# Performance work log

Measured on AMD Instinct MI355X. Metric: run time of the kernel, lower is better.

The kernel has to match this reference:

```python
import jax, jax.numpy as jnp
import numpy as np

INPUT_SIZE = 512
HIDDEN = 1024
NUM_CLASSES = 1000
BATCH = 64
SEQ = 512


def setup_inputs() -> dict:
    key = jax.random.key(0)
    ks = jax.random.split(key, 12)
    comb = INPUT_SIZE + HIDDEN
    s = 1.0 / np.sqrt(comb)
    sf = 1.0 / np.sqrt(HIDDEN)
    return {
        "x": jax.random.normal(ks[0], (BATCH, SEQ, INPUT_SIZE), dtype=jnp.float32),
        "Wz_w": jax.random.uniform(ks[1], (HIDDEN, comb), jnp.float32, -s, s),
        "Wz_b": jax.random.uniform(ks[2], (HIDDEN,), jnp.float32, -s, s),
        "Wr_w": jax.random.uniform(ks[3], (HIDDEN, comb), jnp.float32, -s, s),
        "Wr_b": jax.random.uniform(ks[4], (HIDDEN,), jnp.float32, -s, s),
        "Wc_w": jax.random.uniform(ks[5], (HIDDEN, comb), jnp.float32, -s, s),
        "Wc_b": jax.random.uniform(ks[6], (HIDDEN,), jnp.float32, -s, s),
        "Wo_w": jax.random.uniform(ks[7], (HIDDEN, comb), jnp.float32, -s, s),
        "Wo_b": jax.random.uniform(ks[8], (HIDDEN,), jnp.float32, -s, s),
        "fc_w": jax.random.uniform(ks[9], (NUM_CLASSES, HIDDEN), jnp.float32, -sf, sf),
        "fc_b": jax.random.uniform(ks[10], (NUM_CLASSES,), jnp.float32, -sf, sf),
    }


def reference(x, Wz_w, Wz_b, Wr_w, Wr_b, Wc_w, Wc_b, Wo_w, Wo_b, fc_w, fc_b):
    B, T, _ = x.shape
    H = Wz_w.shape[0]

    def step(carry, x_t):
        h, c = carry
        combined = jnp.concatenate([x_t, h], axis=1)          # [B, I+H]
        z = jax.nn.sigmoid(combined @ Wz_w.T + Wz_b)
        r = jax.nn.sigmoid(combined @ Wr_w.T + Wr_b)
        combined_reset = jnp.concatenate([x_t, r * c], axis=1)
        c_tilde = jnp.tanh(combined_reset @ Wc_w.T + Wc_b)
        c_new = z * c + (1.0 - z) * c_tilde
        o = jax.nn.sigmoid(combined @ Wo_w.T + Wo_b)
        h_new = o * jnp.tanh(c_new)
        return (h_new, c_new), None

    h0 = jnp.zeros((B, H), dtype=x.dtype)
    c0 = jnp.zeros((B, H), dtype=x.dtype)
    xs = jnp.swapaxes(x, 0, 1)                                # [T, B, I]
    (h, c), _ = jax.lax.scan(step, (h0, c0), xs)
    # dropout is identity (p=0 / eval mode)
    return h @ fc_w.T + fc_b                                  # [B, num_classes]
```

## Files before the change

kernel.cpp:

```cpp
#include <hip/hip_runtime.h>

#define NWG 128
#define TSTEPS 512

typedef __attribute__((ext_vector_type(8))) short short8;
typedef __attribute__((ext_vector_type(4))) float f32x4;

#define T0_OFF   0
#define T1_OFF   49152
#define T2_OFF   98304
#define RED_OFF  131072
#define ZBUF_OFF 135168
#define OBUF_OFF 137216
#define XCB_OFF  139264
#define CST_OFF  141312
#define RCS_OFF  143360
#define HST_OFF  145408
#define BIAS_OFF 147456
#define LDS_BYTES 147584

__device__ inline unsigned short f2bf(float f) {
  unsigned int b = __float_as_uint(f);
  return (unsigned short)((b + 0x7FFFu + ((b >> 16) & 1u)) >> 16);
}
__device__ inline float sigm(float x) { return 1.f / (1.f + __expf(-x)); }
__device__ inline float tanh_f(float x) { float e = __expf(2.f * x); return 1.f - 2.f / (e + 1.f); }

__device__ inline void cstore16(void* p, short8 v) {
  asm volatile("global_store_dwordx4 %0, %1, off sc0 sc1" :: "v"(p), "v"(v) : "memory");
}
__device__ inline void cstore4(void* p, int v) {
  asm volatile("global_store_dword %0, %1, off sc0 sc1" :: "v"(p), "v"(v) : "memory");
}
__device__ inline int cload4(const void* p) {
  int v;
  asm volatile("global_load_dword %0, %1, off sc0 sc1\n\ts_waitcnt vmcnt(0)"
               : "=&v"(v) : "v"(p) : "memory");
  return v;
}
__device__ inline void vmdrain() {
  asm volatile("s_waitcnt vmcnt(0)" ::: "memory");
}

__device__ inline void cload24(const unsigned short* p0, const unsigned short* p1, short8* a) {
  asm volatile(
    "global_load_dwordx4 %0,  %24, off sc0 sc1\n\t"
    "global_load_dwordx4 %1,  %24, off offset:64 sc0 sc1\n\t"
    "global_load_dwordx4 %2,  %24, off offset:128 sc0 sc1\n\t"
    "global_load_dwordx4 %3,  %24, off offset:192 sc0 sc1\n\t"
    "global_load_dwordx4 %4,  %24, off offset:256 sc0 sc1\n\t"
    "global_load_dwordx4 %5,  %24, off offset:320 sc0 sc1\n\t"
    "global_load_dwordx4 %6,  %24, off offset:384 sc0 sc1\n\t"
    "global_load_dwordx4 %7,  %24, off offset:448 sc0 sc1\n\t"
    "global_load_dwordx4 %8,  %24, off offset:512 sc0 sc1\n\t"
    "global_load_dwordx4 %9,  %24, off offset:576 sc0 sc1\n\t"
    "global_load_dwordx4 %10, %24, off offset:640 sc0 sc1\n\t"
    "global_load_dwordx4 %11, %24, off offset:704 sc0 sc1\n\t"
    "global_load_dwordx4 %12, %24, off offset:768 sc0 sc1\n\t"
    "global_load_dwordx4 %13, %24, off offset:832 sc0 sc1\n\t"
    "global_load_dwordx4 %14, %24, off offset:896 sc0 sc1\n\t"
    "global_load_dwordx4 %15, %24, off offset:960 sc0 sc1\n\t"
    "global_load_dwordx4 %16, %25, off sc0 sc1\n\t"
    "global_load_dwordx4 %17, %25, off offset:64 sc0 sc1\n\t"
    "global_load_dwordx4 %18, %25, off offset:128 sc0 sc1\n\t"
    "global_load_dwordx4 %19, %25, off offset:192 sc0 sc1\n\t"
    "global_load_dwordx4 %20, %25, off offset:256 sc0 sc1\n\t"
    "global_load_dwordx4 %21, %25, off offset:320 sc0 sc1\n\t"
    "global_load_dwordx4 %22, %25, off offset:384 sc0 sc1\n\t"
    "global_load_dwordx4 %23, %25, off offset:448 sc0 sc1\n\t"
    "s_waitcnt vmcnt(0)"
    : "=&v"(a[0]), "=&v"(a[1]), "=&v"(a[2]), "=&v"(a[3]),
      "=&v"(a[4]), "=&v"(a[5]), "=&v"(a[6]), "=&v"(a[7]),
      "=&v"(a[8]), "=&v"(a[9]), "=&v"(a[10]), "=&v"(a[11]),
      "=&v"(a[12]), "=&v"(a[13]), "=&v"(a[14]), "=&v"(a[15]),
      "=&v"(a[16]), "=&v"(a[17]), "=&v"(a[18]), "=&v"(a[19]),
      "=&v"(a[20]), "=&v"(a[21]), "=&v"(a[22]), "=&v"(a[23])
    : "v"(p0), "v"(p1)
    : "memory");
}

__device__ inline void cload16(const unsigned short* p, short8* a) {
  asm volatile(
    "global_load_dwordx4 %0,  %16, off sc0 sc1\n\t"
    "global_load_dwordx4 %1,  %16, off offset:64 sc0 sc1\n\t"
    "global_load_dwordx4 %2,  %16, off offset:128 sc0 sc1\n\t"
    "global_load_dwordx4 %3,  %16, off offset:192 sc0 sc1\n\t"
    "global_load_dwordx4 %4,  %16, off offset:256 sc0 sc1\n\t"
    "global_load_dwordx4 %5,  %16, off offset:320 sc0 sc1\n\t"
    "global_load_dwordx4 %6,  %16, off offset:384 sc0 sc1\n\t"
    "global_load_dwordx4 %7,  %16, off offset:448 sc0 sc1\n\t"
    "global_load_dwordx4 %8,  %16, off offset:512 sc0 sc1\n\t"
    "global_load_dwordx4 %9,  %16, off offset:576 sc0 sc1\n\t"
    "global_load_dwordx4 %10, %16, off offset:640 sc0 sc1\n\t"
    "global_load_dwordx4 %11, %16, off offset:704 sc0 sc1\n\t"
    "global_load_dwordx4 %12, %16, off offset:768 sc0 sc1\n\t"
    "global_load_dwordx4 %13, %16, off offset:832 sc0 sc1\n\t"
    "global_load_dwordx4 %14, %16, off offset:896 sc0 sc1\n\t"
    "global_load_dwordx4 %15, %16, off offset:960 sc0 sc1\n\t"
    "s_waitcnt vmcnt(0)"
    : "=&v"(a[0]), "=&v"(a[1]), "=&v"(a[2]), "=&v"(a[3]),
      "=&v"(a[4]), "=&v"(a[5]), "=&v"(a[6]), "=&v"(a[7]),
      "=&v"(a[8]), "=&v"(a[9]), "=&v"(a[10]), "=&v"(a[11]),
      "=&v"(a[12]), "=&v"(a[13]), "=&v"(a[14]), "=&v"(a[15])
    : "v"(p)
    : "memory");
}

__global__ void __launch_bounds__(256) lmgru_kernel(
    const float* __restrict__ x,
    const float* __restrict__ Wz, const float* __restrict__ bz,
    const float* __restrict__ Wr, const float* __restrict__ br,
    const float* __restrict__ Wc, const float* __restrict__ bc,
    const float* __restrict__ Wo, const float* __restrict__ bo,
    const float* __restrict__ fcw, const float* __restrict__ fcb,
    float* __restrict__ out, char* __restrict__ ws)
{
  extern __shared__ char lds[];
  const int tid  = threadIdx.x;
  const int wg   = blockIdx.x;
  const int lane = tid & 63;
  const int q    = tid >> 6;

  unsigned short* hbuf  = (unsigned short*)ws;
  unsigned short* rcbuf = (unsigned short*)(ws + 262144);
  unsigned short* xring = (unsigned short*)(ws + 524288);
  float*          h32   = (float*)(ws + 655360);
  int* hflagA  = (int*)(ws + 917504);
  int* hflagB  = hflagA + 128;
  int* rcflagA = hflagA + 256;
  int* rcflagB = hflagA + 384;
  int* hflag[2]  = {hflagA, hflagB};
  int* rcflag[2] = {rcflagA, rcflagB};

  float* zbuf = (float*)(lds + ZBUF_OFF);
  float* obuf = (float*)(lds + OBUF_OFF);
  float* xcb  = (float*)(lds + XCB_OFF);
  float* cst  = (float*)(lds + CST_OFF);
  float* rcs  = (float*)(lds + RCS_OFF);
  float* hst  = (float*)(lds + HST_OFF);
  float* bias = (float*)(lds + BIAS_OFF);

  const float* Wg[4] = {Wz, Wr, Wo, Wc};

  for (int it = 0; it < 12; ++it) {
    int slot = tid + 256 * it;
    int s = slot >> 6, l = slot & 63;
    int nn = l & 15, kg = (l >> 4) & 3;
    int k = 32 * s + kg * 8;
    int g = (nn < 8) ? 0 : 1;
    const float* src = Wg[g] + (8 * wg + (nn & 7)) * 1536 + k;
    short8 pk;
    #pragma unroll
    for (int j = 0; j < 8; ++j) pk[j] = (short)f2bf(src[j]);
    *(short8*)(lds + T0_OFF + s * 1024 + l * 16) = pk;
  }
  for (int it = 0; it < 12; ++it) {
    int slot = tid + 256 * it;
    int s = slot >> 6, l = slot & 63;
    int nn = l & 15, kg = (l >> 4) & 3;
    int k = 32 * s + kg * 8;
    int g = (nn < 8) ? 2 : 3;
    short8 pk = {};
    if (g == 2 || k < 512) {
      const float* src = Wg[g] + (8 * wg + (nn & 7)) * 1536 + k;
      #pragma unroll
      for (int j = 0; j < 8; ++j) pk[j] = (short)f2bf(src[j]);
    }
    *(short8*)(lds + T1_OFF + s * 1024 + l * 16) = pk;
  }
  for (int it = 0; it < 8; ++it) {
    int slot = tid + 256 * it;
    int s = slot >> 6, l = slot & 63;
    int nn = l & 15, kg = (l >> 4) & 3;
    int k = 32 * s + kg * 8;
    short8 pk = {};
    if (nn < 8) {
      const float* src = Wc + (8 * wg + nn) * 1536 + 512 + k;
      #pragma unroll
      for (int j = 0; j < 8; ++j) pk[j] = (short)f2bf(src[j]);
    }
    *(short8*)(lds + T2_OFF + s * 1024 + l * 16) = pk;
  }
  if (tid < 32) {
    const float* Bg[4] = {bz, br, bo, bc};
    bias[tid] = Bg[tid >> 3][8 * wg + (tid & 7)];
  }
  cst[tid] = 0.f; cst[tid + 256] = 0.f;
  if (tid < 64) {
    short8 z8 = {};
    cstore16(hbuf + tid * 1024 + 8 * wg, z8);
  }
  if (tid < 32) {
    int e = wg * 256 + tid * 8;
    int b = e >> 9, f = e & 511;
    const float* xs = x + b * 262144 + f;
    short8 pk;
    #pragma unroll
    for (int j = 0; j < 8; ++j) pk[j] = (short)f2bf(xs[j]);
    cstore16(xring + 32768 + b * 512 + f, pk);
  }
  __syncthreads();
  if (tid == 0) {
    vmdrain();
    cstore4(&hflagA[wg], 0);
    cstore4(&hflagB[wg], 0);
    cstore4(&rcflagA[wg], 0);
    cstore4(&rcflagB[wg], 0);
  }

  const int m   = q & 1;
  const int kh  = q >> 1;
  const int nn  = lane & 15;
  const int kg8 = ((lane >> 4) & 3) * 8;
  const int rbase = ((lane >> 4) & 3) * 4;

  for (int t = 1; t <= TSTEPS; ++t) {
    const int pc = t & 1, pp = (t - 1) & 1;

    for (int X = 0; X < 2; ++X) {
      if (tid < 128) {
        const int* fp = &hflag[X][tid];
        while (cload4(fp) < t - 1) __builtin_amdgcn_s_sleep(1);
      }
      __syncthreads();

      const int bbase = 32 * X;
      const int brow  = bbase + 16 * m + nn;
      f32x4 acc0 = {0.f, 0.f, 0.f, 0.f}, acc1 = {0.f, 0.f, 0.f, 0.f};
      const unsigned short* xr = xring + pc * 32768 + brow * 512;
      const unsigned short* hb = hbuf + pp * 65536 + brow * 1024;
      const unsigned short* p0 = kh ? (hb + 256 + kg8) : (xr + kg8);
      const unsigned short* p1 = kh ? (hb + 768 + kg8) : (hb + kg8);
      short8 af[24];
      cload24(p0, p1, af);
      #pragma unroll
      for (int j = 0; j < 24; ++j) {
        int s = 24 * kh + j;
        short8 b0 = *(const short8*)(lds + T0_OFF + s * 1024 + lane * 16);
        short8 b1 = *(const short8*)(lds + T1_OFF + s * 1024 + lane * 16);
        acc0 = __builtin_amdgcn_mfma_f32_16x16x32_bf16(af[j], b0, acc0, 0, 0, 0);
        acc1 = __builtin_amdgcn_mfma_f32_16x16x32_bf16(af[j], b1, acc1, 0, 0, 0);
      }
      if (kh == 1) {
        *(f32x4*)(lds + RED_OFF + ((m * 2 + 0) * 64 + lane) * 16) = acc0;
        *(f32x4*)(lds + RED_OFF + ((m * 2 + 1) * 64 + lane) * 16) = acc1;
      }
      __syncthreads();
      if (kh == 0) {
        acc0 += *(const f32x4*)(lds + RED_OFF + ((m * 2 + 0) * 64 + lane) * 16);
        acc1 += *(const f32x4*)(lds + RED_OFF + ((m * 2 + 1) * 64 + lane) * 16);
        #pragma unroll
        for (int i = 0; i < 4; ++i) {
          int b = bbase + 16 * m + rbase + i;
          float v0 = acc0[i] + bias[nn];
          float v1 = acc1[i] + bias[16 + nn];
          if (nn < 8) {
            zbuf[nn * 64 + b] = sigm(v0);
            obuf[nn * 64 + b] = sigm(v1);
          } else {
            int u = nn - 8;
            rcs[u * 64 + b] = sigm(v0) * cst[u * 64 + b];
            xcb[u * 64 + b] = v1;
          }
        }
      }
      __syncthreads();
      if (tid < 32) {
        int b = bbase + tid;
        short8 pk;
        #pragma unroll
        for (int u = 0; u < 8; ++u) pk[u] = (short)f2bf(rcs[u * 64 + b]);
        cstore16(rcbuf + pc * 65536 + b * 1024 + 8 * wg, pk);
      }
      if (tid == 0) {
        vmdrain();
        cstore4(&rcflag[X][wg], t);
      }
    }

    for (int X = 0; X < 2; ++X) {
      if (tid < 128) {
        const int* fp = &rcflag[X][tid];
        while (cload4(fp) < t) __builtin_amdgcn_s_sleep(1);
      }
      __syncthreads();

      const int bbase = 32 * X;
      const int brow  = bbase + 16 * m + nn;
      f32x4 acc = {0.f, 0.f, 0.f, 0.f};
      const unsigned short* rb = rcbuf + pc * 65536 + brow * 1024;
      short8 af[16];
      cload16(rb + kg8 + (kh ? 512 : 0), af);
      #pragma unroll
      for (int j = 0; j < 16; ++j) {
        int s = 16 * kh + j;
        short8 bf = *(const short8*)(lds + T2_OFF + s * 1024 + lane * 16);
        acc = __builtin_amdgcn_mfma_f32_16x16x32_bf16(af[j], bf, acc, 0, 0, 0);
      }
      if (kh == 1) *(f32x4*)(lds + RED_OFF + (m * 64 + lane) * 16) = acc;
      __syncthreads();
      if (kh == 0 && nn < 8) {
        acc += *(const f32x4*)(lds + RED_OFF + (m * 64 + lane) * 16);
        #pragma unroll
        for (int i = 0; i < 4; ++i) {
          int b = bbase + 16 * m + rbase + i;
          float ct = tanh_f(acc[i] + xcb[nn * 64 + b]);
          float z  = zbuf[nn * 64 + b];
          float cn = z * cst[nn * 64 + b] + (1.f - z) * ct;
          cst[nn * 64 + b] = cn;
          hst[nn * 64 + b] = obuf[nn * 64 + b] * tanh_f(cn);
        }
      }
      __syncthreads();
      if (tid < 32) {
        int b = bbase + tid;
        if (t < TSTEPS) {
          short8 pk;
          #pragma unroll
          for (int u = 0; u < 8; ++u) pk[u] = (short)f2bf(hst[u * 64 + b]);
          cstore16(hbuf + pc * 65536 + b * 1024 + 8 * wg, pk);
        } else {
          #pragma unroll
          for (int u = 0; u < 8; ++u) h32[b * 1024 + 8 * wg + u] = hst[u * 64 + b];
        }
      }
      if (X == 0 && t < TSTEPS && tid < 32) {
        int e = wg * 256 + tid * 8;
        int b = e >> 9, f = e & 511;
        const float* xs = x + b * 262144 + t * 512 + f;
        short8 pk;
        #pragma unroll
        for (int j = 0; j < 8; ++j) pk[j] = (short)f2bf(xs[j]);
        cstore16(xring + ((t + 1) & 1) * 32768 + b * 512 + f, pk);
      }
      if (tid == 0) {
        if (t < TSTEPS) {
          vmdrain();
          cstore4(&hflag[X][wg], t);
        } else {
          __hip_atomic_store(&hflag[X][wg], t, __ATOMIC_RELEASE, __HIP_MEMORY_SCOPE_AGENT);
        }
      }
    }
  }

  if (tid < 128) {
    while (__hip_atomic_load(&hflagA[tid], __ATOMIC_RELAXED, __HIP_MEMORY_SCOPE_AGENT) < TSTEPS)
      __builtin_amdgcn_s_sleep(1);
    while (__hip_atomic_load(&hflagB[tid], __ATOMIC_RELAXED, __HIP_MEMORY_SCOPE_AGENT) < TSTEPS)
      __builtin_amdgcn_s_sleep(1);
  }
  __syncthreads();
  __builtin_amdgcn_fence(__ATOMIC_ACQUIRE, "agent");

  if (wg < 125) {
    for (int cc = 0; cc < 2; ++cc) {
      int c = 8 * wg + 2 * q + cc;
      const float* wrow = fcw + c * 1024;
      for (int b = 0; b < 64; ++b) {
        const float* hrow = h32 + b * 1024;
        float s = 0.f;
        for (int kk = lane; kk < 1024; kk += 64) s = __builtin_fmaf(hrow[kk], wrow[kk], s);
        #pragma unroll
        for (int off = 32; off; off >>= 1) s += __shfl_xor(s, off);
        if (lane == 0) out[b * 1000 + c] = s + fcb[c];
      }
    }
  }
}

extern "C" void kernel_launch(void* const* d_in, const int* in_sizes, int n_in,
                              void* d_out, int out_size, void* d_ws, size_t ws_size,
                              hipStream_t stream) {
  (void)in_sizes; (void)n_in; (void)out_size; (void)ws_size;
  const float* x   = (const float*)d_in[0];
  const float* Wz  = (const float*)d_in[1];
  const float* bz  = (const float*)d_in[2];
  const float* Wr  = (const float*)d_in[3];
  const float* br  = (const float*)d_in[4];
  const float* Wc  = (const float*)d_in[5];
  const float* bc  = (const float*)d_in[6];
  const float* Wo  = (const float*)d_in[7];
  const float* bo  = (const float*)d_in[8];
  const float* fcw = (const float*)d_in[9];
  const float* fcb = (const float*)d_in[10];

  hipFuncSetAttribute((const void*)lmgru_kernel,
                      hipFuncAttributeMaxDynamicSharedMemorySize, LDS_BYTES);

  hipLaunchKernelGGL(lmgru_kernel, dim3(NWG), dim3(256), LDS_BYTES, stream,
                     x, Wz, bz, Wr, br, Wc, bc, Wo, bo, fcw, fcb,
                     (float*)d_out, (char*)d_ws);
}
```

Before: 9.934 ms.

## Load x directly per step and overlap its MFMA with h wait; pad flags and LDS

Removes the bf16 x ring buffer and instead has each wave read x from global fp32, converting it with packed bf16 cvt before spinning on the h flags. The x-part MFMAs then run while the h loads are in flight, taking the input projection off the inter-workgroup critical path. Flags are spaced 64 bytes apart so each sits on its own line, and the LDS gate buffers use a 65-float stride to avoid bank conflicts. The cost is more global fp32 traffic per step and higher register pressure from the axf/xv arrays.

```diff
diff --git a/kernel.cpp b/kernel.cpp
--- a/kernel.cpp
+++ b/kernel.cpp
@@ -5,19 +5,21 @@
 
 typedef __attribute__((ext_vector_type(8))) short short8;
 typedef __attribute__((ext_vector_type(4))) float f32x4;
+typedef __attribute__((ext_vector_type(4))) int int4v;
 
 #define T0_OFF   0
 #define T1_OFF   49152
 #define T2_OFF   98304
 #define RED_OFF  131072
 #define ZBUF_OFF 135168
-#define OBUF_OFF 137216
-#define XCB_OFF  139264
-#define CST_OFF  141312
-#define RCS_OFF  143360
-#define HST_OFF  145408
-#define BIAS_OFF 147456
-#define LDS_BYTES 147584
+#define OBUF_OFF 137248
+#define XCB_OFF  139328
+#define CST_OFF  141408
+#define RCS_OFF  143488
+#define HST_OFF  145568
+#define BIAS_OFF 147648
+#define LDS_BYTES 147776
+#define PAD 65
 
 __device__ inline unsigned short f2bf(float f) {
   unsigned int b = __float_as_uint(f);
@@ -25,6 +27,16 @@
 }
 __device__ inline float sigm(float x) { return 1.f / (1.f + __expf(-x)); }
 __device__ inline float tanh_f(float x) { float e = __expf(2.f * x); return 1.f - 2.f / (e + 1.f); }
+
+__device__ inline short8 cvt8(f32x4 a, f32x4 b) {
+  int w0, w1, w2, w3;
+  asm("v_cvt_pk_bf16_f32 %0, %1, %2" : "=v"(w0) : "v"(a[0]), "v"(a[1]));
+  asm("v_cvt_pk_bf16_f32 %0, %1, %2" : "=v"(w1) : "v"(a[2]), "v"(a[3]));
+  asm("v_cvt_pk_bf16_f32 %0, %1, %2" : "=v"(w2) : "v"(b[0]), "v"(b[1]));
+  asm("v_cvt_pk_bf16_f32 %0, %1, %2" : "=v"(w3) : "v"(b[2]), "v"(b[3]));
+  int4v r = {w0, w1, w2, w3};
+  return __builtin_bit_cast(short8, r);
+}
 
 __device__ inline void cstore16(void* p, short8 v) {
   asm volatile("global_store_dwordx4 %0, %1, off sc0 sc1" :: "v"(p), "v"(v) : "memory");
@@ -40,43 +52,6 @@
 }
 __device__ inline void vmdrain() {
   asm volatile("s_waitcnt vmcnt(0)" ::: "memory");
-}
-
-__device__ inline void cload24(const unsigned short* p0, const unsigned short* p1, short8* a) {
-  asm volatile(
-    "global_load_dwordx4 %0,  %24, off sc0 sc1\n\t"
-    "global_load_dwordx4 %1,  %24, off offset:64 sc0 sc1\n\t"
-    "global_load_dwordx4 %2,  %24, off offset:128 sc0 sc1\n\t"
-    "global_load_dwordx4 %3,  %24, off offset:192 sc0 sc1\n\t"
-    "global_load_dwordx4 %4,  %24, off offset:256 sc0 sc1\n\t"
-    "global_load_dwordx4 %5,  %24, off offset:320 sc0 sc1\n\t"
-    "global_load_dwordx4 %6,  %24, off offset:384 sc0 sc1\n\t"
-    "global_load_dwordx4 %7,  %24, off offset:448 sc0 sc1\n\t"
-    "global_load_dwordx4 %8,  %24, off offset:512 sc0 sc1\n\t"
-    "global_load_dwordx4 %9,  %24, off offset:576 sc0 sc1\n\t"
-    "global_load_dwordx4 %10, %24, off offset:640 sc0 sc1\n\t"
-    "global_load_dwordx4 %11, %24, off offset:704 sc0 sc1\n\t"
-    "global_load_dwordx4 %12, %24, off offset:768 sc0 sc1\n\t"
-    "global_load_dwordx4 %13, %24, off offset:832 sc0 sc1\n\t"
-    "global_load_dwordx4 %14, %24, off offset:896 sc0 sc1\n\t"
-    "global_load_dwordx4 %15, %24, off offset:960 sc0 sc1\n\t"
-    "global_load_dwordx4 %16, %25, off sc0 sc1\n\t"
-    "global_load_dwordx4 %17, %25, off offset:64 sc0 sc1\n\t"
-    "global_load_dwordx4 %18, %25, off offset:128 sc0 sc1\n\t"
-    "global_load_dwordx4 %19, %25, off offset:192 sc0 sc1\n\t"
-    "global_load_dwordx4 %20, %25, off offset:256 sc0 sc1\n\t"
-    "global_load_dwordx4 %21, %25, off offset:320 sc0 sc1\n\t"
-    "global_load_dwordx4 %22, %25, off offset:384 sc0 sc1\n\t"
-    "global_load_dwordx4 %23, %25, off offset:448 sc0 sc1\n\t"
-    "s_waitcnt vmcnt(0)"
-    : "=&v"(a[0]), "=&v"(a[1]), "=&v"(a[2]), "=&v"(a[3]),
-      "=&v"(a[4]), "=&v"(a[5]), "=&v"(a[6]), "=&v"(a[7]),
-      "=&v"(a[8]), "=&v"(a[9]), "=&v"(a[10]), "=&v"(a[11]),
-      "=&v"(a[12]), "=&v"(a[13]), "=&v"(a[14]), "=&v"(a[15]),
-      "=&v"(a[16]), "=&v"(a[17]), "=&v"(a[18]), "=&v"(a[19]),
-      "=&v"(a[20]), "=&v"(a[21]), "=&v"(a[22]), "=&v"(a[23])
-    : "v"(p0), "v"(p1)
-    : "memory");
 }
 
 __device__ inline void cload16(const unsigned short* p, short8* a) {
@@ -106,7 +81,33 @@
     : "memory");
 }
 
-__global__ void __launch_bounds__(256) lmgru_kernel(
+__device__ inline void cload16_issue(const unsigned short* p, short8* a) {
+  asm volatile(
+    "global_load_dwordx4 %0,  %16, off sc0 sc1\n\t"
+    "global_load_dwordx4 %1,  %16, off offset:64 sc0 sc1\n\t"
+    "global_load_dwordx4 %2,  %16, off offset:128 sc0 sc1\n\t"
+    "global_load_dwordx4 %3,  %16, off offset:192 sc0 sc1\n\t"
+    "global_load_dwordx4 %4,  %16, off offset:256 sc0 sc1\n\t"
+    "global_load_dwordx4 %5,  %16, off offset:320 sc0 sc1\n\t"
+    "global_load_dwordx4 %6,  %16, off offset:384 sc0 sc1\n\t"
+    "global_load_dwordx4 %7,  %16, off offset:448 sc0 sc1\n\t"
+    "global_load_dwordx4 %8,  %16, off offset:512 sc0 sc1\n\t"
+    "global_load_dwordx4 %9,  %16, off offset:576 sc0 sc1\n\t"
+    "global_load_dwordx4 %10, %16, off offset:640 sc0 sc1\n\t"
+    "global_load_dwordx4 %11, %16, off offset:704 sc0 sc1\n\t"
+    "global_load_dwordx4 %12, %16, off offset:768 sc0 sc1\n\t"
+    "global_load_dwordx4 %13, %16, off offset:832 sc0 sc1\n\t"
+    "global_load_dwordx4 %14, %16, off offset:896 sc0 sc1\n\t"
+    "global_load_dwordx4 %15, %16, off offset:960 sc0 sc1"
+    : "=&v"(a[0]), "=&v"(a[1]), "=&v"(a[2]), "=&v"(a[3]),
+      "=&v"(a[4]), "=&v"(a[5]), "=&v"(a[6]), "=&v"(a[7]),
+      "=&v"(a[8]), "=&v"(a[9]), "=&v"(a[10]), "=&v"(a[11]),
+      "=&v"(a[12]), "=&v"(a[13]), "=&v"(a[14]), "=&v"(a[15])
+    : "v"(p)
+    : "memory");
+}
+
+__global__ void __launch_bounds__(256, 1) lmgru_kernel(
     const float* __restrict__ x,
     const float* __restrict__ Wz, const float* __restrict__ bz,
     const float* __restrict__ Wr, const float* __restrict__ br,
@@ -123,12 +124,11 @@
 
   unsigned short* hbuf  = (unsigned short*)ws;
   unsigned short* rcbuf = (unsigned short*)(ws + 262144);
-  unsigned short* xring = (unsigned short*)(ws + 524288);
   float*          h32   = (float*)(ws + 655360);
-  int* hflagA  = (int*)(ws + 917504);
-  int* hflagB  = hflagA + 128;
-  int* rcflagA = hflagA + 256;
-  int* rcflagB = hflagA + 384;
+  int* hflagA  = (int*)(ws + 524288);
+  int* hflagB  = hflagA + 2048;
+  int* rcflagA = hflagA + 4096;
+  int* rcflagB = hflagA + 6144;
   int* hflag[2]  = {hflagA, hflagB};
   int* rcflag[2] = {rcflagA, rcflagB};
 
@@ -185,27 +185,18 @@
     const float* Bg[4] = {bz, br, bo, bc};
     bias[tid] = Bg[tid >> 3][8 * wg + (tid & 7)];
   }
-  cst[tid] = 0.f; cst[tid + 256] = 0.f;
+  for (int i2 = tid; i2 < 8 * PAD; i2 += 256) cst[i2] = 0.f;
   if (tid < 64) {
     short8 z8 = {};
     cstore16(hbuf + tid * 1024 + 8 * wg, z8);
   }
-  if (tid < 32) {
-    int e = wg * 256 + tid * 8;
-    int b = e >> 9, f = e & 511;
-    const float* xs = x + b * 262144 + f;
-    short8 pk;
-    #pragma unroll
-    for (int j = 0; j < 8; ++j) pk[j] = (short)f2bf(xs[j]);
-    cstore16(xring + 32768 + b * 512 + f, pk);
-  }
   __syncthreads();
   if (tid == 0) {
     vmdrain();
-    cstore4(&hflagA[wg], 0);
-    cstore4(&hflagB[wg], 0);
-    cstore4(&rcflagA[wg], 0);
-    cstore4(&rcflagB[wg], 0);
+    cstore4(hflagA + wg * 16, 0);
+    cstore4(hflagB + wg * 16, 0);
+    cstore4(rcflagA + wg * 16, 0);
+    cstore4(rcflagB + wg * 16, 0);
   }
 
   const int m   = q & 1;
@@ -218,28 +209,56 @@
     const int pc = t & 1, pp = (t - 1) & 1;
 
     for (int X = 0; X < 2; ++X) {
-      if (tid < 128) {
-        const int* fp = &hflag[X][tid];
-        while (cload4(fp) < t - 1) __builtin_amdgcn_s_sleep(1);
-      }
-      __syncthreads();
-
       const int bbase = 32 * X;
       const int brow  = bbase + 16 * m + nn;
+
+      short8 axf[16];
+      if (kh == 0) {
+        const float* xp = x + brow * 262144 + (t - 1) * 512 + kg8;
+        #pragma unroll
+        for (int c = 0; c < 2; ++c) {
+          f32x4 xv[16];
+          #pragma unroll
+          for (int j = 0; j < 8; ++j) {
+            xv[2 * j]     = *(const f32x4*)(xp + 32 * (8 * c + j));
+            xv[2 * j + 1] = *(const f32x4*)(xp + 32 * (8 * c + j) + 4);
+          }
+          #pragma unroll
+          for (int j = 0; j < 8; ++j) axf[8 * c + j] = cvt8(xv[2 * j], xv[2 * j + 1]);
+        }
+      }
+
+      if (tid < 128) {
+        const int* fp = hflag[X] + tid * 16;
+        while (cload4(fp) < t - 1) __builtin_amdgcn_s_sleep(1);
+      }
+      __syncthreads();
+
       f32x4 acc0 = {0.f, 0.f, 0.f, 0.f}, acc1 = {0.f, 0.f, 0.f, 0.f};
-      const unsigned short* xr = xring + pc * 32768 + brow * 512;
       const unsigned short* hb = hbuf + pp * 65536 + brow * 1024;
-      const unsigned short* p0 = kh ? (hb + 256 + kg8) : (xr + kg8);
-      const unsigned short* p1 = kh ? (hb + 768 + kg8) : (hb + kg8);
-      short8 af[24];
-      cload24(p0, p1, af);
-      #pragma unroll
-      for (int j = 0; j < 24; ++j) {
-        int s = 24 * kh + j;
-        short8 b0 = *(const short8*)(lds + T0_OFF + s * 1024 + lane * 16);
-        short8 b1 = *(const short8*)(lds + T1_OFF + s * 1024 + lane * 16);
-        acc0 = __builtin_amdgcn_mfma_f32_16x16x32_bf16(af[j], b0, acc0, 0, 0, 0);
-        acc1 = __builtin_amdgcn_mfma_f32_16x16x32_bf16(af[j], b1, acc1, 0, 0, 0);
+      short8 ah[16];
+      cload16_issue(hb + (kh ? 512 : 0) + kg8, ah);
+      if (kh == 0) {
+        #pragma unroll
+        for (int j = 0; j < 16; ++j) {
+          short8 b0 = *(const short8*)(lds + T0_OFF + j * 1024 + lane * 16);
+          short8 b1 = *(const short8*)(lds + T1_OFF + j * 1024 + lane * 16);
+          acc0 = __builtin_amdgcn_mfma_f32_16x16x32_bf16(axf[j], b0, acc0, 0, 0, 0);
+          acc1 = __builtin_amdgcn_mfma_f32_16x16x32_bf16(axf[j], b1, acc1, 0, 0, 0);
+        }
+      }
+      vmdrain();
+      __builtin_amdgcn_sched_barrier(0);
+      {
+        const int sb = kh ? 32 : 16;
+        #pragma unroll
+        for (int j = 0; j < 16; ++j) {
+          int s = sb + j;
+          short8 b0 = *(const short8*)(lds + T0_OFF + s * 1024 + lane * 16);
+          short8 b1 = *(const short8*)(lds + T1_OFF + s * 1024 + lane * 16);
+          acc0 = __builtin_amdgcn_mfma_f32_16x16x32_bf16(ah[j], b0, acc0, 0, 0, 0);
+          acc1 = __builtin_amdgcn_mfma_f32_16x16x32_bf16(ah[j], b1, acc1, 0, 0, 0);
+        }
       }
       if (kh == 1) {
         *(f32x4*)(lds + RED_OFF + ((m * 2 + 0) * 64 + lane) * 16) = acc0;
@@ -255,12 +274,12 @@
           float v0 = acc0[i] + bias[nn];
           float v1 = acc1[i] + bias[16 + nn];
           if (nn < 8) {
-            zbuf[nn * 64 + b] = sigm(v0);
-            obuf[nn * 64 + b] = sigm(v1);
+            zbuf[nn * PAD + b] = sigm(v0);
+            obuf[nn * PAD + b] = sigm(v1);
           } else {
             int u = nn - 8;
-            rcs[u * 64 + b] = sigm(v0) * cst[u * 64 + b];
-            xcb[u * 64 + b] = v1;
+            rcs[u * PAD + b] = sigm(v0) * cst[u * PAD + b];
+            xcb[u * PAD + b] = v1;
           }
         }
       }
@@ -269,18 +288,18 @@
         int b = bbase + tid;
         short8 pk;
         #pragma unroll
-        for (int u = 0; u < 8; ++u) pk[u] = (short)f2bf(rcs[u * 64 + b]);
+        for (int u = 0; u < 8; ++u) pk[u] = (short)f2bf(rcs[u * PAD + b]);
         cstore16(rcbuf + pc * 65536 + b * 1024 + 8 * wg, pk);
       }
       if (tid == 0) {
         vmdrain();
-        cstore4(&rcflag[X][wg], t);
+        cstore4(rcflag[X] + wg * 16, t);
       }
     }
 
     for (int X = 0; X < 2; ++X) {
       if (tid < 128) {
-        const int* fp = &rcflag[X][tid];
+        const int* fp = rcflag[X] + tid * 16;
         while (cload4(fp) < t) __builtin_amdgcn_s_sleep(1);
       }
       __syncthreads();
@@ -304,11 +323,11 @@
         #pragma unroll
         for (int i = 0; i < 4; ++i) {
           int b = bbase + 16 * m + rbase + i;
-          float ct = tanh_f(acc[i] + xcb[nn * 64 + b]);
-          float z  = zbuf[nn * 64 + b];
-          float cn = z * cst[nn * 64 + b] + (1.f - z) * ct;
-          cst[nn * 64 + b] = cn;
-          hst[nn * 64 + b] = obuf[nn * 64 + b] * tanh_f(cn);
+          float ct = tanh_f(acc[i] + xcb[nn * PAD + b]);
+          float z  = zbuf[nn * PAD + b];
+          float cn = z * cst[nn * PAD + b] + (1.f - z) * ct;
+          cst[nn * PAD + b] = cn;
+          hst[nn * PAD + b] = obuf[nn * PAD + b] * tanh_f(cn);
         }
       }
       __syncthreads();
@@ -317,37 +336,28 @@
         if (t < TSTEPS) {
           short8 pk;
           #pragma unroll
-          for (int u = 0; u < 8; ++u) pk[u] = (short)f2bf(hst[u * 64 + b]);
+          for (int u = 0; u < 8; ++u) pk[u] = (short)f2bf(hst[u * PAD + b]);
           cstore16(hbuf + pc * 65536 + b * 1024 + 8 * wg, pk);
         } else {
           #pragma unroll
-          for (int u = 0; u < 8; ++u) h32[b * 1024 + 8 * wg + u] = hst[u * 64 + b];
-        }
-      }
-      if (X == 0 && t < TSTEPS && tid < 32) {
-        int e = wg * 256 + tid * 8;
-        int b = e >> 9, f = e & 511;
-        const float* xs = x + b * 262144 + t * 512 + f;
-        short8 pk;
-        #pragma unroll
-        for (int j = 0; j < 8; ++j) pk[j] = (short)f2bf(xs[j]);
-        cstore16(xring + ((t + 1) & 1) * 32768 + b * 512 + f, pk);
+          for (int u = 0; u < 8; ++u) h32[b * 1024 + 8 * wg + u] = hst[u * PAD + b];
+        }
       }
       if (tid == 0) {
         if (t < TSTEPS) {
           vmdrain();
-          cstore4(&hflag[X][wg], t);
+          cstore4(hflag[X] + wg * 16, t);
         } else {
-          __hip_atomic_store(&hflag[X][wg], t, __ATOMIC_RELEASE, __HIP_MEMORY_SCOPE_AGENT);
+          __hip_atomic_store(hflag[X] + wg * 16, t, __ATOMIC_RELEASE, __HIP_MEMORY_SCOPE_AGENT);
         }
       }
     }
   }
 
   if (tid < 128) {
-    while (__hip_atomic_load(&hflagA[tid], __ATOMIC_RELAXED, __HIP_MEMORY_SCOPE_AGENT) < TSTEPS)
+    while (__hip_atomic_load(hflagA + tid * 16, __ATOMIC_RELAXED, __HIP_MEMORY_SCOPE_AGENT) < TSTEPS)
       __builtin_amdgcn_s_sleep(1);
-    while (__hip_atomic_load(&hflagB[tid], __ATOMIC_RELAXED, __HIP_MEMORY_SCOPE_AGENT) < TSTEPS)
+    while (__hip_atomic_load(hflagB + tid * 16, __ATOMIC_RELAXED, __HIP_MEMORY_SCOPE_AGENT) < TSTEPS)
       __builtin_amdgcn_s_sleep(1);
   }
   __syncthreads();
```

After: 10.88 ms. 9.5% more time.
